# Kernel optimization log

Measured on AMD Instinct MI355X. Metric: run time of the kernel, lower is better.

The kernel has to match this reference:

```python
import jax, jax.numpy as jnp
import numpy as np

N_NODES = 50000
N_EDGES = 1600000
IN_DIM = 128
HEADS = 8
OUT_C = 16  # per-head channels; HEADS*OUT_C == IN_DIM -> residual active
NEG_SLOPE = 0.2
BN_EPS = 1e-5


def setup_inputs() -> dict:
    key = jax.random.key(0)
    ks = jax.random.split(key, 8)
    x = jax.random.normal(ks[0], (N_NODES, IN_DIM), dtype=jnp.float32)
    edge_index = jax.random.randint(ks[1], (2, N_EDGES), 0, N_NODES, dtype=jnp.int64)
    # GATConv params (PyG: shared lin for src/dst on single-tensor input)
    W = jax.random.normal(ks[2], (IN_DIM, HEADS * OUT_C), dtype=jnp.float32) / np.sqrt(IN_DIM)
    att_src = jax.random.normal(ks[3], (HEADS, OUT_C), dtype=jnp.float32) / np.sqrt(OUT_C)
    att_dst = jax.random.normal(ks[4], (HEADS, OUT_C), dtype=jnp.float32) / np.sqrt(OUT_C)
    bias = jnp.zeros((HEADS * OUT_C,), dtype=jnp.float32)
    # BatchNorm1d affine params
    gamma = jnp.ones((HEADS * OUT_C,), dtype=jnp.float32)
    beta = jnp.zeros((HEADS * OUT_C,), dtype=jnp.float32)
    return {"x": x, "edge_index": edge_index, "W": W, "att_src": att_src,
            "att_dst": att_dst, "bias": bias, "gamma": gamma, "beta": beta}


def reference(x, edge_index, W, att_src, att_dst, bias, gamma, beta):
    N = x.shape[0]
    H, C = att_src.shape
    src, dst = edge_index[0], edge_index[1]

    xl = (x @ W).reshape(N, H, C)                      # [N,H,C]
    a_src = jnp.sum(xl * att_src[None], axis=-1)       # [N,H]
    a_dst = jnp.sum(xl * att_dst[None], axis=-1)       # [N,H]

    e = jax.nn.leaky_relu(a_src[src] + a_dst[dst], NEG_SLOPE)  # [E,H]
    # segment softmax over incoming edges of each dst node
    m = jax.ops.segment_max(e, dst, num_segments=N)    # [N,H], -inf for empty
    m = jnp.where(jnp.isfinite(m), m, 0.0)
    ex = jnp.exp(e - m[dst])                           # [E,H]
    denom = jax.ops.segment_sum(ex, dst, num_segments=N)
    alpha = ex / (denom[dst] + 1e-16)                  # [E,H]

    out = jax.ops.segment_sum(alpha[:, :, None] * xl[src], dst, num_segments=N)  # [N,H,C]
    h = out.reshape(N, H * C) + bias

    # BatchNorm1d (training mode: batch statistics, biased variance)
    mean = jnp.mean(h, axis=0)
    var = jnp.mean((h - mean) ** 2, axis=0)
    h = (h - mean) * jax.lax.rsqrt(var + BN_EPS) * gamma + beta

    h = jax.nn.relu(h)
    return x + h  # residual (in_dim == H*C)
```

## Files before the change

kernel.cpp:

```cpp
#include <hip/hip_runtime.h>
#include <hip/hip_fp16.h>
#include <math.h>

#define N_NODES 50000
#define N_EDGES 1600000
#define DIM 128
#define HEADS 8
#define NEG_SLOPE 0.2f
#define BN_EPS 1e-5f

typedef _Float16 f16x8 __attribute__((ext_vector_type(8)));
typedef float f32x4 __attribute__((ext_vector_type(4)));

#define NBUCK 196
#define SEGCAP 12288
#define CHUNK 8192
#define NB_A ((N_EDGES + CHUNK - 1) / CHUNK)
#define LIN_NB ((N_NODES + 127) / 128)
#define FUSED_NB (NB_A + LIN_NB)

struct BinAShm {
    int hist[NBUCK], excl[NBUCK], gbase[NBUCK], cnt2[NBUCK];
    int sc[256];
    unsigned int buf[CHUNK];
};
struct LinShm { __half wh[16384]; };

__global__ __launch_bounds__(512) void k_linbinA(
        const float* __restrict__ x, const float* __restrict__ W,
        const float* __restrict__ att_s, const float* __restrict__ att_d,
        const int* __restrict__ ei, int* __restrict__ bcur,
        unsigned int* __restrict__ pairs, __half* __restrict__ xlh,
        float* __restrict__ a_src, float* __restrict__ a_dst) {
    __shared__ union { BinAShm a; LinShm l; } sh;
    const int t = threadIdx.x;

    if (blockIdx.x < NB_A) {
        const int base = blockIdx.x * CHUNK;
        const int cnt = min(CHUNK, N_EDGES - base);

        for (int j = t; j < NBUCK; j += 512) { sh.a.hist[j] = 0; sh.a.cnt2[j] = 0; }
        __syncthreads();
        for (int i = t * 4; i < cnt; i += 2048) {
            const int4 dv = *(const int4*)(ei + N_EDGES + base + i);
            atomicAdd(&sh.a.hist[dv.x >> 8], 1);
            atomicAdd(&sh.a.hist[dv.y >> 8], 1);
            atomicAdd(&sh.a.hist[dv.z >> 8], 1);
            atomicAdd(&sh.a.hist[dv.w >> 8], 1);
        }
        __syncthreads();
        if (t < 256) sh.a.sc[t] = (t < NBUCK) ? sh.a.hist[t] : 0;
        __syncthreads();
        for (int d = 1; d < 256; d <<= 1) {
            int xo = 0;
            if (t < 256 && t >= d) xo = sh.a.sc[t - d];
            __syncthreads();
            if (t < 256) sh.a.sc[t] += xo;
            __syncthreads();
        }
        if (t < NBUCK) {
            sh.a.excl[t] = sh.a.sc[t] - sh.a.hist[t];
            sh.a.gbase[t] = t * SEGCAP + atomicAdd(&bcur[t], sh.a.hist[t]);
        }
        __syncthreads();
        for (int i = t * 4; i < cnt; i += 2048) {
            const int4 sv = *(const int4*)(ei + base + i);
            const int4 dv = *(const int4*)(ei + N_EDGES + base + i);
            const int ss[4] = {sv.x, sv.y, sv.z, sv.w};
            const int dd[4] = {dv.x, dv.y, dv.z, dv.w};
            #pragma unroll
            for (int k = 0; k < 4; ++k) {
                const int b = dd[k] >> 8;
                const int r = atomicAdd(&sh.a.cnt2[b], 1);
                sh.a.buf[sh.a.excl[b] + r] = (unsigned int)ss[k]
                    | ((unsigned int)(dd[k] & 255) << 16) | ((unsigned int)b << 24);
            }
        }
        __syncthreads();
        for (int i = t; i < cnt; i += 512) {
            const unsigned int u = sh.a.buf[i];
            const int b = u >> 24;
            pairs[sh.a.gbase[b] + (i - sh.a.excl[b])] = u & 0xFFFFFF;
        }
    } else {
        for (int v = t; v < 2048; v += 512) {
            const int g = v >> 6, lane = v & 63;
            const int nt = g >> 2, kt = g & 3;
            const int q = lane >> 4, n = lane & 15;
            #pragma unroll
            for (int j = 0; j < 8; ++j)
                sh.l.wh[(size_t)(g * 64 + lane) * 8 + j] =
                    __float2half(W[(kt * 32 + q * 8 + j) * DIM + nt * 16 + n]);
        }
        __syncthreads();

        const int wave = t >> 6;
        const int lane = t & 63;
        const int q = lane >> 4, n = lane & 15;
        const int nb = ((blockIdx.x - NB_A) * 8 + wave) * 16;

        const int rowA = min(nb + n, N_NODES - 1);
        const float* xr = x + (size_t)rowA * DIM;
        f16x8 a[4];
        #pragma unroll
        for (int kt = 0; kt < 4; ++kt) {
            const float4 p0 = *(const float4*)(xr + kt * 32 + q * 8);
            const float4 p1 = *(const float4*)(xr + kt * 32 + q * 8 + 4);
            a[kt][0] = (_Float16)p0.x; a[kt][1] = (_Float16)p0.y;
            a[kt][2] = (_Float16)p0.z; a[kt][3] = (_Float16)p0.w;
            a[kt][4] = (_Float16)p1.x; a[kt][5] = (_Float16)p1.y;
            a[kt][6] = (_Float16)p1.z; a[kt][7] = (_Float16)p1.w;
        }

        f32x4 acc[8];
        #pragma unroll
        for (int nt = 0; nt < 8; ++nt) acc[nt] = (f32x4){0.f, 0.f, 0.f, 0.f};

        const f16x8* wb = (const f16x8*)sh.l.wh;
        #pragma unroll
        for (int nt = 0; nt < 8; ++nt) {
            #pragma unroll
            for (int kt = 0; kt < 4; ++kt) {
                const f16x8 b = wb[(nt * 4 + kt) * 64 + lane];
                acc[nt] = __builtin_amdgcn_mfma_f32_16x16x32_f16(a[kt], b, acc[nt], 0, 0, 0);
            }
        }

        const int r0 = nb + q * 4;
        #pragma unroll
        for (int nt = 0; nt < 8; ++nt) {
            const float as = att_s[nt * 16 + n];
            const float ad = att_d[nt * 16 + n];
            #pragma unroll
            for (int r = 0; r < 4; ++r) {
                const int row = r0 + r;
                const float v = acc[nt][r];
                float s = v * as;
                float d = v * ad;
                #pragma unroll
                for (int off = 8; off; off >>= 1) {
                    s += __shfl_xor(s, off, 16);
                    d += __shfl_xor(d, off, 16);
                }
                if (row < N_NODES) {
                    xlh[(size_t)row * DIM + nt * 16 + n] = __float2half(v);
                    if (n == 0) {
                        a_src[row * HEADS + nt] = s * 1.44269504f;
                        a_dst[row * HEADS + nt] = d * 1.44269504f;
                    }
                }
            }
        }
    }
}

__global__ __launch_bounds__(1024) void k_binB(const unsigned int* __restrict__ pairs,
                                               const int* __restrict__ bcur,
                                               unsigned short* __restrict__ csr,
                                               int2* __restrict__ nrange,
                                               float* __restrict__ gsums) {
    __shared__ int hist[256], eh[256], excl[256], cnt2[256];
    __shared__ int plen;
    __shared__ unsigned short out[SEGCAP];
    const int t = threadIdx.x;
    const int b = blockIdx.x;
    if (b == 0 && t < 256) gsums[t] = 0.f;
    const int lo = b * SEGCAP;
    const int cnt = bcur[b];

    if (t < 256) { hist[t] = 0; cnt2[t] = 0; }
    __syncthreads();
    for (int i = t; i < cnt; i += 1024)
        atomicAdd(&hist[pairs[lo + i] >> 16], 1);
    __syncthreads();
    if (t < 256) { eh[t] = (hist[t] + 1) & ~1; excl[t] = eh[t]; }
    __syncthreads();
    for (int d = 1; d < 256; d <<= 1) {
        int xo = 0;
        if (t < 256 && t >= d) xo = excl[t - d];
        __syncthreads();
        if (t < 256) excl[t] += xo;
        __syncthreads();
    }
    if (t < 256) excl[t] -= eh[t];
    if (t == 255) plen = excl[255] + eh[255];
    __syncthreads();
    for (int i = t; i < cnt; i += 1024) {
        const unsigned int u = pairs[lo + i];
        const int dl = u >> 16;
        const int r = atomicAdd(&cnt2[dl], 1);
        out[excl[dl] + r] = (unsigned short)(u & 0xFFFF);
    }
    __syncthreads();
    const int pl = plen;
    for (int i = t; i < pl; i += 1024)
        csr[2 * lo + i] = out[i];
    if (t < 256) {
        const int node = (b << 8) + t;
        if (node < N_NODES) {
            int2 rg;
            rg.x = 2 * lo + excl[t];
            rg.y = rg.x + hist[t];
            nrange[node] = rg;
        }
    }
}

#define AGG_NB (N_NODES / 4)

__global__ void k_aggr9(const int2* __restrict__ nrange,
                        const unsigned short* __restrict__ csr,
                        const float* __restrict__ a_src, const float* __restrict__ a_dst,
                        const __half* __restrict__ xlh, float* __restrict__ y) {
    const int d = blockIdx.x * 4 + (threadIdx.x >> 6);
    const int lane = threadIdx.x & 63;
    const int g = lane >> 4;
    const int cl = lane & 15;
    const int h = cl >> 1;
    const int2 rg = nrange[d];
    const int lo = rg.x, hi = rg.y;
    const float ad = a_dst[d * HEADS + h];

    float acc[8];
    #pragma unroll
    for (int k = 0; k < 8; ++k) acc[k] = 0.f;
    float dsum = 0.f;

    int i = lo;
    for (; i + 16 <= hi; i += 16) {
        const int s0 = csr[i + g];
        const int s1 = csr[i + 4 + g];
        const int s2 = csr[i + 8 + g];
        const int s3 = csr[i + 12 + g];
        const float as0 = a_src[s0 * HEADS + h];
        const float as1 = a_src[s1 * HEADS + h];
        const float as2 = a_src[s2 * HEADS + h];
        const float as3 = a_src[s3 * HEADS + h];
        const f16x8 x0 = *(const f16x8*)(xlh + (size_t)s0 * DIM + cl * 8);
        const f16x8 x1 = *(const f16x8*)(xlh + (size_t)s1 * DIM + cl * 8);
        const f16x8 x2 = *(const f16x8*)(xlh + (size_t)s2 * DIM + cl * 8);
        const f16x8 x3 = *(const f16x8*)(xlh + (size_t)s3 * DIM + cl * 8);
        const float e0 = as0 + ad;
        const float e1 = as1 + ad;
        const float e2 = as2 + ad;
        const float e3 = as3 + ad;
        const float w0 = exp2f(fmaxf(e0, NEG_SLOPE * e0));
        const float w1 = exp2f(fmaxf(e1, NEG_SLOPE * e1));
        const float w2 = exp2f(fmaxf(e2, NEG_SLOPE * e2));
        const float w3 = exp2f(fmaxf(e3, NEG_SLOPE * e3));
        dsum += (w0 + w1) + (w2 + w3);
        #pragma unroll
        for (int k = 0; k < 8; ++k) acc[k] = fmaf(w0, (float)x0[k], acc[k]);
        #pragma unroll
        for (int k = 0; k < 8; ++k) acc[k] = fmaf(w1, (float)x1[k], acc[k]);
        #pragma unroll
        for (int k = 0; k < 8; ++k) acc[k] = fmaf(w2, (float)x2[k], acc[k]);
        #pragma unroll
        for (int k = 0; k < 8; ++k) acc[k] = fmaf(w3, (float)x3[k], acc[k]);
    }
    for (; i + 8 <= hi; i += 8) {
        const int s0 = csr[i + g];
        const int s1 = csr[i + 4 + g];
        const float as0 = a_src[s0 * HEADS + h];
        const float as1 = a_src[s1 * HEADS + h];
        const f16x8 x0 = *(const f16x8*)(xlh + (size_t)s0 * DIM + cl * 8);
        const f16x8 x1 = *(const f16x8*)(xlh + (size_t)s1 * DIM + cl * 8);
        const float e0 = as0 + ad;
        const float e1 = as1 + ad;
        const float w0 = exp2f(fmaxf(e0, NEG_SLOPE * e0));
        const float w1 = exp2f(fmaxf(e1, NEG_SLOPE * e1));
        dsum += w0 + w1;
        #pragma unroll
        for (int k = 0; k < 8; ++k) acc[k] = fmaf(w0, (float)x0[k], acc[k]);
        #pragma unroll
        for (int k = 0; k < 8; ++k) acc[k] = fmaf(w1, (float)x1[k], acc[k]);
    }
    for (; i < hi; i += 4) {
        const int idx = i + g;
        const int sv = csr[min(idx, hi - 1)];
        const float e = a_src[sv * HEADS + h] + ad;
        const f16x8 xv = *(const f16x8*)(xlh + (size_t)sv * DIM + cl * 8);
        float w = exp2f(fmaxf(e, NEG_SLOPE * e));
        if (idx >= hi) w = 0.f;
        dsum += w;
        #pragma unroll
        for (int k = 0; k < 8; ++k) acc[k] = fmaf(w, (float)xv[k], acc[k]);
    }
    #pragma unroll
    for (int k = 0; k < 8; ++k) {
        acc[k] += __shfl_xor(acc[k], 16);
        acc[k] += __shfl_xor(acc[k], 32);
    }
    dsum += __shfl_xor(dsum, 16);
    dsum += __shfl_xor(dsum, 32);
    const float inv = 1.f / (dsum + 1e-16f);
    float2 o;
    o.x = acc[2 * g] * inv;
    o.y = acc[2 * g + 1] * inv;
    *(float2*)(y + (size_t)d * DIM + cl * 8 + g * 2) = o;
}

__global__ void k_stats(const float* __restrict__ y, const float* __restrict__ bias,
                        float* __restrict__ gsums) {
    const int c = threadIdx.x;
    const float b = bias[c];
    float s = 0.f, ss = 0.f;
    for (int n = blockIdx.x; n < N_NODES; n += gridDim.x) {
        const float h = y[n * DIM + c] + b;
        s += h;
        ss += h * h;
    }
    atomicAdd(&gsums[c], s);
    atomicAdd(&gsums[DIM + c], ss);
}

__global__ void k_final(float* __restrict__ y, const float* __restrict__ x,
                        const float* __restrict__ sums, const float* __restrict__ sumsq,
                        const float* __restrict__ gamma, const float* __restrict__ beta,
                        const float* __restrict__ bias) {
    const int q = blockIdx.x * blockDim.x + threadIdx.x;
    const int cq = q & (DIM / 4 - 1);
    const float4 sm = ((const float4*)sums)[cq];
    const float4 sq = ((const float4*)sumsq)[cq];
    const float4 gm = ((const float4*)gamma)[cq];
    const float4 bt = ((const float4*)beta)[cq];
    const float4 bs = ((const float4*)bias)[cq];
    float4 v = ((const float4*)y)[q];
    const float4 xv = ((const float4*)x)[q];
    const float inv_n = 1.f / (float)N_NODES;
#define BNC(c) { const float mean = sm.c * inv_n;                         \
                 const float var = sq.c * inv_n - mean * mean;            \
                 const float sc = rsqrtf(var + BN_EPS) * gm.c;            \
                 const float sh = bt.c + (bs.c - mean) * sc;              \
                 v.c = xv.c + fmaxf(v.c * sc + sh, 0.f); }
    BNC(x) BNC(y) BNC(z) BNC(w)
#undef BNC
    ((float4*)y)[q] = v;
}

extern "C" void kernel_launch(void* const* d_in, const int* in_sizes, int n_in,
                              void* d_out, int out_size, void* d_ws, size_t ws_size,
                              hipStream_t stream) {
    const float* x     = (const float*)d_in[0];
    const int*   ei    = (const int*)  d_in[1];
    const float* W     = (const float*)d_in[2];
    const float* att_s = (const float*)d_in[3];
    const float* att_d = (const float*)d_in[4];
    const float* bias  = (const float*)d_in[5];
    const float* gamma = (const float*)d_in[6];
    const float* beta  = (const float*)d_in[7];
    float* y = (float*)d_out;

    __half* xlh  = (__half*)d_ws;
    float* a_src = (float*)(xlh + (size_t)N_NODES * DIM);
    float* a_dst = a_src + (size_t)N_NODES * HEADS;
    float* sums  = a_dst + (size_t)N_NODES * HEADS;
    float* sumsq = sums  + DIM;
    int*   bcur  = (int*)(sumsq + DIM);
    int2*  nrange = (int2*)(bcur + 256);
    unsigned int* pairs = (unsigned int*)(nrange + N_NODES);
    unsigned short* csr = (unsigned short*)pairs;

    hipMemsetAsync(bcur, 0, 256 * sizeof(int), stream);
    k_linbinA<<<FUSED_NB, 512, 0, stream>>>(x, W, att_s, att_d, ei, bcur, pairs,
                                            xlh, a_src, a_dst);
    k_binB<<<NBUCK, 1024, 0, stream>>>(pairs, bcur, csr, nrange, sums);
    k_aggr9<<<AGG_NB, 256, 0, stream>>>(nrange, csr, a_src, a_dst, xlh, y);
    k_stats<<<512, DIM, 0, stream>>>(y, bias, sums);
    k_final<<<(size_t)N_NODES * DIM / 4 / 256, 256, 0, stream>>>(y, x, sums, sumsq,
                                                                 gamma, beta, bias);
}
```

Measured before the change: 229.2 us.

## Compute per-node degrees globally and scatter CSR directly without LDS staging

The bin-A pass now also counts per-destination degrees with global atomics. The second binning kernel uses those degrees and a bucket prefix scan to build a compact CSR, and scatters source ids straight to global memory through LDS cursors. This replaces the LDS histogram, the padded output buffer and the copy-out. In exchange it adds 1.6M global atomics, a larger memset, and uncoalesced global scatter writes. It also drops the even-padding of segments, which k_aggr9 may assume, and shrinks SEGCAP, which risks overflow if a bucket gets more edges than that.

```diff
diff --git a/kernel.cpp b/kernel.cpp
--- a/kernel.cpp
+++ b/kernel.cpp
@@ -13,7 +13,7 @@
 typedef float f32x4 __attribute__((ext_vector_type(4)));
 
 #define NBUCK 196
-#define SEGCAP 12288
+#define SEGCAP 9216
 #define CHUNK 8192
 #define NB_A ((N_EDGES + CHUNK - 1) / CHUNK)
 #define LIN_NB ((N_NODES + 127) / 128)
@@ -30,6 +30,7 @@
         const float* __restrict__ x, const float* __restrict__ W,
         const float* __restrict__ att_s, const float* __restrict__ att_d,
         const int* __restrict__ ei, int* __restrict__ bcur,
+        int* __restrict__ deg,
         unsigned int* __restrict__ pairs, __half* __restrict__ xlh,
         float* __restrict__ a_src, float* __restrict__ a_dst) {
     __shared__ union { BinAShm a; LinShm l; } sh;
@@ -47,6 +48,10 @@
             atomicAdd(&sh.a.hist[dv.y >> 8], 1);
             atomicAdd(&sh.a.hist[dv.z >> 8], 1);
             atomicAdd(&sh.a.hist[dv.w >> 8], 1);
+            atomicAdd(&deg[dv.x], 1);
+            atomicAdd(&deg[dv.y], 1);
+            atomicAdd(&deg[dv.z], 1);
+            atomicAdd(&deg[dv.w], 1);
         }
         __syncthreads();
         if (t < 256) sh.a.sc[t] = (t < NBUCK) ? sh.a.hist[t] : 0;
@@ -154,55 +159,61 @@
     }
 }
 
-__global__ __launch_bounds__(1024) void k_binB(const unsigned int* __restrict__ pairs,
+__global__ __launch_bounds__(512) void k_binB2(const unsigned int* __restrict__ pairs,
                                                const int* __restrict__ bcur,
+                                               const int* __restrict__ deg,
                                                unsigned short* __restrict__ csr,
                                                int2* __restrict__ nrange,
                                                float* __restrict__ gsums) {
-    __shared__ int hist[256], eh[256], excl[256], cnt2[256];
-    __shared__ int plen;
-    __shared__ unsigned short out[SEGCAP];
+    __shared__ int bsc[256];
+    __shared__ int dsc[256];
+    __shared__ int cur[256];
     const int t = threadIdx.x;
     const int b = blockIdx.x;
     if (b == 0 && t < 256) gsums[t] = 0.f;
-    const int lo = b * SEGCAP;
-    const int cnt = bcur[b];
-
-    if (t < 256) { hist[t] = 0; cnt2[t] = 0; }
-    __syncthreads();
-    for (int i = t; i < cnt; i += 1024)
-        atomicAdd(&hist[pairs[lo + i] >> 16], 1);
-    __syncthreads();
-    if (t < 256) { eh[t] = (hist[t] + 1) & ~1; excl[t] = eh[t]; }
+
+    if (t < 256) bsc[t] = (t < NBUCK) ? bcur[t] : 0;
     __syncthreads();
     for (int d = 1; d < 256; d <<= 1) {
         int xo = 0;
-        if (t < 256 && t >= d) xo = excl[t - d];
-        __syncthreads();
-        if (t < 256) excl[t] += xo;
-        __syncthreads();
-    }
-    if (t < 256) excl[t] -= eh[t];
-    if (t == 255) plen = excl[255] + eh[255];
+        if (t < 256 && t >= d) xo = bsc[t - d];
+        __syncthreads();
+        if (t < 256) bsc[t] += xo;
+        __syncthreads();
+    }
+    const int boff = (b == 0) ? 0 : bsc[b - 1];
+
+    int dg = 0;
+    const int node = (b << 8) + t;
+    if (t < 256) {
+        dg = (node < N_NODES) ? deg[node] : 0;
+        dsc[t] = dg;
+    }
     __syncthreads();
-    for (int i = t; i < cnt; i += 1024) {
+    for (int d = 1; d < 256; d <<= 1) {
+        int xo = 0;
+        if (t < 256 && t >= d) xo = dsc[t - d];
+        __syncthreads();
+        if (t < 256) dsc[t] += xo;
+        __syncthreads();
+    }
+    if (t < 256) {
+        const int start = boff + dsc[t] - dg;
+        if (node < N_NODES) {
+            int2 rg; rg.x = start; rg.y = start + dg;
+            nrange[node] = rg;
+        }
+        cur[t] = start;
+    }
+    __syncthreads();
+
+    const int cnt = bcur[b];
+    const int lo = b * SEGCAP;
+    for (int i = t; i < cnt; i += 512) {
         const unsigned int u = pairs[lo + i];
-        const int dl = u >> 16;
-        const int r = atomicAdd(&cnt2[dl], 1);
-        out[excl[dl] + r] = (unsigned short)(u & 0xFFFF);
-    }
-    __syncthreads();
-    const int pl = plen;
-    for (int i = t; i < pl; i += 1024)
-        csr[2 * lo + i] = out[i];
-    if (t < 256) {
-        const int node = (b << 8) + t;
-        if (node < N_NODES) {
-            int2 rg;
-            rg.x = 2 * lo + excl[t];
-            rg.y = rg.x + hist[t];
-            nrange[node] = rg;
-        }
+        const int dl = (u >> 16) & 255;
+        const int pos = atomicAdd(&cur[dl], 1);
+        csr[pos] = (unsigned short)(u & 0xFFFF);
     }
 }
 
@@ -356,15 +367,16 @@
     float* a_dst = a_src + (size_t)N_NODES * HEADS;
     float* sums  = a_dst + (size_t)N_NODES * HEADS;
     float* sumsq = sums  + DIM;
-    int*   bcur  = (int*)(sumsq + DIM);
+    int*   deg   = (int*)(sumsq + DIM);
+    int*   bcur  = deg + N_NODES;
     int2*  nrange = (int2*)(bcur + 256);
     unsigned int* pairs = (unsigned int*)(nrange + N_NODES);
-    unsigned short* csr = (unsigned short*)pairs;
-
-    hipMemsetAsync(bcur, 0, 256 * sizeof(int), stream);
-    k_linbinA<<<FUSED_NB, 512, 0, stream>>>(x, W, att_s, att_d, ei, bcur, pairs,
-                                            xlh, a_src, a_dst);
-    k_binB<<<NBUCK, 1024, 0, stream>>>(pairs, bcur, csr, nrange, sums);
+    unsigned short* csr = (unsigned short*)(pairs + (size_t)NBUCK * SEGCAP);
+
+    hipMemsetAsync(sums, 0, (size_t)(2 * DIM + N_NODES + 256) * sizeof(int), stream);
+    k_linbinA<<<FUSED_NB, 512, 0, stream>>>(x, W, att_s, att_d, ei, bcur, deg,
+                                            pairs, xlh, a_src, a_dst);
+    k_binB2<<<NBUCK, 512, 0, stream>>>(pairs, bcur, deg, csr, nrange, sums);
     k_aggr9<<<AGG_NB, 256, 0, stream>>>(nrange, csr, a_src, a_dst, xlh, y);
     k_stats<<<512, DIM, 0, stream>>>(y, bias, sums);
     k_final<<<(size_t)N_NODES * DIM / 4 / 256, 256, 0, stream>>>(y, x, sums, sumsq,
```

Result: slower. 288.8 us (+26.0%).

## Replace global bucket atomics with per-chunk metadata and split linear work across phases

Applied to the files above, without the earlier changes.

Binning pass A now writes each chunk's bucket-sorted pairs contiguously with per-chunk histogram/offset metadata, instead of scattering through global atomic cursors. Pass B gathers each bucket's pieces from all chunks via a prefix sum plus binary search. The memset and the global atomics go away. The linear/MFMA blocks are split across both phases so the second binning kernel overlaps with part of the GEMM work. The trade-off is extra metadata traffic, binary-search cost per edge in phase 2, and the lost CSR padding alignment.

```diff
diff --git a/kernel.cpp b/kernel.cpp
--- a/kernel.cpp
+++ b/kernel.cpp
@@ -17,29 +17,114 @@
 #define CHUNK 8192
 #define NB_A ((N_EDGES + CHUNK - 1) / CHUNK)
 #define LIN_NB ((N_NODES + 127) / 128)
-#define FUSED_NB (NB_A + LIN_NB)
+#define LIN_K1 195
+#define LIN_K2 (LIN_NB - LIN_K1)
+#define P1_NB (NB_A + LIN_K1)
+#define P2_NB (NBUCK + LIN_K2)
 
 struct BinAShm {
-    int hist[NBUCK], excl[NBUCK], gbase[NBUCK], cnt2[NBUCK];
+    int hist[NBUCK], excl[NBUCK], cnt2[NBUCK];
     int sc[256];
     unsigned int buf[CHUNK];
 };
+struct BinBShm {
+    int la[256], ea[256], rs[256];
+    int hist[256], excl[256], cnt2[256], sc[256];
+    unsigned short out[SEGCAP];
+};
 struct LinShm { __half wh[16384]; };
 
-__global__ __launch_bounds__(512) void k_linbinA(
+__device__ __forceinline__ void lin_block(
+        int linb, const float* __restrict__ x, const float* __restrict__ W,
+        const float* __restrict__ att_s, const float* __restrict__ att_d,
+        __half* __restrict__ xlh, float* __restrict__ a_src,
+        float* __restrict__ a_dst, __half* wh) {
+    const int t = threadIdx.x;
+    for (int v = t; v < 2048; v += 512) {
+        const int g = v >> 6, lane = v & 63;
+        const int nt = g >> 2, kt = g & 3;
+        const int q = lane >> 4, n = lane & 15;
+        #pragma unroll
+        for (int j = 0; j < 8; ++j)
+            wh[(size_t)(g * 64 + lane) * 8 + j] =
+                __float2half(W[(kt * 32 + q * 8 + j) * DIM + nt * 16 + n]);
+    }
+    __syncthreads();
+
+    const int wave = t >> 6;
+    const int lane = t & 63;
+    const int q = lane >> 4, n = lane & 15;
+    const int nb = (linb * 8 + wave) * 16;
+
+    const int rowA = min(nb + n, N_NODES - 1);
+    const float* xr = x + (size_t)rowA * DIM;
+    f16x8 a[4];
+    #pragma unroll
+    for (int kt = 0; kt < 4; ++kt) {
+        const float4 p0 = *(const float4*)(xr + kt * 32 + q * 8);
+        const float4 p1 = *(const float4*)(xr + kt * 32 + q * 8 + 4);
+        a[kt][0] = (_Float16)p0.x; a[kt][1] = (_Float16)p0.y;
+        a[kt][2] = (_Float16)p0.z; a[kt][3] = (_Float16)p0.w;
+        a[kt][4] = (_Float16)p1.x; a[kt][5] = (_Float16)p1.y;
+        a[kt][6] = (_Float16)p1.z; a[kt][7] = (_Float16)p1.w;
+    }
+
+    f32x4 acc[8];
+    #pragma unroll
+    for (int nt = 0; nt < 8; ++nt) acc[nt] = (f32x4){0.f, 0.f, 0.f, 0.f};
+
+    const f16x8* wb = (const f16x8*)wh;
+    #pragma unroll
+    for (int nt = 0; nt < 8; ++nt) {
+        #pragma unroll
+        for (int kt = 0; kt < 4; ++kt) {
+            const f16x8 b = wb[(nt * 4 + kt) * 64 + lane];
+            acc[nt] = __builtin_amdgcn_mfma_f32_16x16x32_f16(a[kt], b, acc[nt], 0, 0, 0);
+        }
+    }
+
+    const int r0 = nb + q * 4;
+    #pragma unroll
+    for (int nt = 0; nt < 8; ++nt) {
+        const float as = att_s[nt * 16 + n];
+        const float ad = att_d[nt * 16 + n];
+        #pragma unroll
+        for (int r = 0; r < 4; ++r) {
+            const int row = r0 + r;
+            const float v = acc[nt][r];
+            float s = v * as;
+            float d = v * ad;
+            #pragma unroll
+            for (int off = 8; off; off >>= 1) {
+                s += __shfl_xor(s, off, 16);
+                d += __shfl_xor(d, off, 16);
+            }
+            if (row < N_NODES) {
+                xlh[(size_t)row * DIM + nt * 16 + n] = __float2half(v);
+                if (n == 0) {
+                    a_src[row * HEADS + nt] = s * 1.44269504f;
+                    a_dst[row * HEADS + nt] = d * 1.44269504f;
+                }
+            }
+        }
+    }
+}
+
+__global__ __launch_bounds__(512) void k_phase1(
         const float* __restrict__ x, const float* __restrict__ W,
         const float* __restrict__ att_s, const float* __restrict__ att_d,
-        const int* __restrict__ ei, int* __restrict__ bcur,
+        const int* __restrict__ ei, unsigned int* __restrict__ meta,
         unsigned int* __restrict__ pairs, __half* __restrict__ xlh,
         float* __restrict__ a_src, float* __restrict__ a_dst) {
     __shared__ union { BinAShm a; LinShm l; } sh;
     const int t = threadIdx.x;
 
     if (blockIdx.x < NB_A) {
-        const int base = blockIdx.x * CHUNK;
+        const int blk = blockIdx.x;
+        const int base = blk * CHUNK;
         const int cnt = min(CHUNK, N_EDGES - base);
 
-        for (int j = t; j < NBUCK; j += 512) { sh.a.hist[j] = 0; sh.a.cnt2[j] = 0; }
+        if (t < NBUCK) { sh.a.hist[t] = 0; sh.a.cnt2[t] = 0; }
         __syncthreads();
         for (int i = t * 4; i < cnt; i += 2048) {
             const int4 dv = *(const int4*)(ei + N_EDGES + base + i);
@@ -59,8 +144,10 @@
             __syncthreads();
         }
         if (t < NBUCK) {
-            sh.a.excl[t] = sh.a.sc[t] - sh.a.hist[t];
-            sh.a.gbase[t] = t * SEGCAP + atomicAdd(&bcur[t], sh.a.hist[t]);
+            const int ex = sh.a.sc[t] - sh.a.hist[t];
+            sh.a.excl[t] = ex;
+            meta[(size_t)blk * NBUCK + t] =
+                (unsigned int)sh.a.hist[t] | ((unsigned int)ex << 16);
         }
         __syncthreads();
         for (int i = t * 4; i < cnt; i += 2048) {
@@ -73,136 +160,102 @@
                 const int b = dd[k] >> 8;
                 const int r = atomicAdd(&sh.a.cnt2[b], 1);
                 sh.a.buf[sh.a.excl[b] + r] = (unsigned int)ss[k]
-                    | ((unsigned int)(dd[k] & 255) << 16) | ((unsigned int)b << 24);
-            }
-        }
-        __syncthreads();
+                    | ((unsigned int)(dd[k] & 255) << 16);
+            }
+        }
+        __syncthreads();
+        for (int i = t * 4; i < cnt; i += 2048)
+            *(int4*)(pairs + base + i) = *(const int4*)(sh.a.buf + i);
+    } else {
+        lin_block(blockIdx.x - NB_A, x, W, att_s, att_d, xlh, a_src, a_dst, sh.l.wh);
+    }
+}
+
+__global__ __launch_bounds__(512) void k_phase2(
+        const unsigned int* __restrict__ pairs, const unsigned int* __restrict__ meta,
+        unsigned short* __restrict__ csr, int2* __restrict__ nrange,
+        float* __restrict__ gsums,
+        const float* __restrict__ x, const float* __restrict__ W,
+        const float* __restrict__ att_s, const float* __restrict__ att_d,
+        __half* __restrict__ xlh, float* __restrict__ a_src,
+        float* __restrict__ a_dst) {
+    __shared__ union { BinBShm b; LinShm l; } sh;
+    const int t = threadIdx.x;
+
+    if (blockIdx.x < NBUCK) {
+        const int b = blockIdx.x;
+        if (b == 0 && t < 256) gsums[t] = 0.f;
+
+        if (t < 256) {
+            int len = 0, off = 0;
+            if (t < NB_A) {
+                const unsigned int m = meta[(size_t)t * NBUCK + b];
+                len = (int)(m & 0xFFFF);
+                off = (int)(m >> 16);
+            }
+            sh.b.la[t] = len; sh.b.ea[t] = off; sh.b.rs[t] = len;
+            sh.b.hist[t] = 0; sh.b.cnt2[t] = 0;
+        }
+        __syncthreads();
+        for (int d = 1; d < 256; d <<= 1) {
+            int xo = 0;
+            if (t < 256 && t >= d) xo = sh.b.rs[t - d];
+            __syncthreads();
+            if (t < 256) sh.b.rs[t] += xo;
+            __syncthreads();
+        }
+        const int cnt = sh.b.rs[NB_A - 1];
+
         for (int i = t; i < cnt; i += 512) {
-            const unsigned int u = sh.a.buf[i];
-            const int b = u >> 24;
-            pairs[sh.a.gbase[b] + (i - sh.a.excl[b])] = u & 0xFFFFFF;
+            int loa = 0, hia = NB_A - 1;
+            while (loa < hia) {
+                const int mid = (loa + hia) >> 1;
+                if (sh.b.rs[mid] > i) hia = mid; else loa = mid + 1;
+            }
+            const int j = i - (sh.b.rs[loa] - sh.b.la[loa]);
+            const unsigned int u = pairs[(size_t)loa * CHUNK + sh.b.ea[loa] + j];
+            atomicAdd(&sh.b.hist[(u >> 16) & 255], 1);
+        }
+        __syncthreads();
+        if (t < 256) sh.b.sc[t] = sh.b.hist[t];
+        __syncthreads();
+        for (int d = 1; d < 256; d <<= 1) {
+            int xo = 0;
+            if (t < 256 && t >= d) xo = sh.b.sc[t - d];
+            __syncthreads();
+            if (t < 256) sh.b.sc[t] += xo;
+            __syncthreads();
+        }
+        if (t < 256) sh.b.excl[t] = sh.b.sc[t] - sh.b.hist[t];
+        __syncthreads();
+
+        for (int i = t; i < cnt; i += 512) {
+            int loa = 0, hia = NB_A - 1;
+            while (loa < hia) {
+                const int mid = (loa + hia) >> 1;
+                if (sh.b.rs[mid] > i) hia = mid; else loa = mid + 1;
+            }
+            const int j = i - (sh.b.rs[loa] - sh.b.la[loa]);
+            const unsigned int u = pairs[(size_t)loa * CHUNK + sh.b.ea[loa] + j];
+            const int dl = (u >> 16) & 255;
+            const int r = atomicAdd(&sh.b.cnt2[dl], 1);
+            sh.b.out[sh.b.excl[dl] + r] = (unsigned short)(u & 0xFFFF);
+        }
+        __syncthreads();
+        for (int i = t; i < cnt; i += 512)
+            csr[(size_t)b * SEGCAP + i] = sh.b.out[i];
+        if (t < 256) {
+            const int node = (b << 8) + t;
+            if (node < N_NODES) {
+                int2 rg;
+                rg.x = b * SEGCAP + sh.b.excl[t];
+                rg.y = rg.x + sh.b.hist[t];
+                nrange[node] = rg;
+            }
         }
     } else {
-        for (int v = t; v < 2048; v += 512) {
-            const int g = v >> 6, lane = v & 63;
-            const int nt = g >> 2, kt = g & 3;
-            const int q = lane >> 4, n = lane & 15;
-            #pragma unroll
-            for (int j = 0; j < 8; ++j)
-                sh.l.wh[(size_t)(g * 64 + lane) * 8 + j] =
-                    __float2half(W[(kt * 32 + q * 8 + j) * DIM + nt * 16 + n]);
-        }
-        __syncthreads();
-
-        const int wave = t >> 6;
-        const int lane = t & 63;
-        const int q = lane >> 4, n = lane & 15;
-        const int nb = ((blockIdx.x - NB_A) * 8 + wave) * 16;
-
-        const int rowA = min(nb + n, N_NODES - 1);
-        const float* xr = x + (size_t)rowA * DIM;
-        f16x8 a[4];
-        #pragma unroll
-        for (int kt = 0; kt < 4; ++kt) {
-            const float4 p0 = *(const float4*)(xr + kt * 32 + q * 8);
-            const float4 p1 = *(const float4*)(xr + kt * 32 + q * 8 + 4);
-            a[kt][0] = (_Float16)p0.x; a[kt][1] = (_Float16)p0.y;
-            a[kt][2] = (_Float16)p0.z; a[kt][3] = (_Float16)p0.w;
-            a[kt][4] = (_Float16)p1.x; a[kt][5] = (_Float16)p1.y;
-            a[kt][6] = (_Float16)p1.z; a[kt][7] = (_Float16)p1.w;
-        }
-
-        f32x4 acc[8];
-        #pragma unroll
-        for (int nt = 0; nt < 8; ++nt) acc[nt] = (f32x4){0.f, 0.f, 0.f, 0.f};
-
-        const f16x8* wb = (const f16x8*)sh.l.wh;
-        #pragma unroll
-        for (int nt = 0; nt < 8; ++nt) {
-            #pragma unroll
-            for (int kt = 0; kt < 4; ++kt) {
-                const f16x8 b = wb[(nt * 4 + kt) * 64 + lane];
-                acc[nt] = __builtin_amdgcn_mfma_f32_16x16x32_f16(a[kt], b, acc[nt], 0, 0, 0);
-            }
-        }
-
-        const int r0 = nb + q * 4;
-        #pragma unroll
-        for (int nt = 0; nt < 8; ++nt) {
-            const float as = att_s[nt * 16 + n];
-            const float ad = att_d[nt * 16 + n];
-            #pragma unroll
-            for (int r = 0; r < 4; ++r) {
-                const int row = r0 + r;
-                const float v = acc[nt][r];
-                float s = v * as;
-                float d = v * ad;
-                #pragma unroll
-                for (int off = 8; off; off >>= 1) {
-                    s += __shfl_xor(s, off, 16);
-                    d += __shfl_xor(d, off, 16);
-                }
-                if (row < N_NODES) {
-                    xlh[(size_t)row * DIM + nt * 16 + n] = __float2half(v);
-                    if (n == 0) {
-                        a_src[row * HEADS + nt] = s * 1.44269504f;
-                        a_dst[row * HEADS + nt] = d * 1.44269504f;
-                    }
-                }
-            }
-        }
-    }
-}
-
-__global__ __launch_bounds__(1024) void k_binB(const unsigned int* __restrict__ pairs,
-                                               const int* __restrict__ bcur,
-                                               unsigned short* __restrict__ csr,
-                                               int2* __restrict__ nrange,
-                                               float* __restrict__ gsums) {
-    __shared__ int hist[256], eh[256], excl[256], cnt2[256];
-    __shared__ int plen;
-    __shared__ unsigned short out[SEGCAP];
-    const int t = threadIdx.x;
-    const int b = blockIdx.x;
-    if (b == 0 && t < 256) gsums[t] = 0.f;
-    const int lo = b * SEGCAP;
-    const int cnt = bcur[b];
-
-    if (t < 256) { hist[t] = 0; cnt2[t] = 0; }
-    __syncthreads();
-    for (int i = t; i < cnt; i += 1024)
-        atomicAdd(&hist[pairs[lo + i] >> 16], 1);
-    __syncthreads();
-    if (t < 256) { eh[t] = (hist[t] + 1) & ~1; excl[t] = eh[t]; }
-    __syncthreads();
-    for (int d = 1; d < 256; d <<= 1) {
-        int xo = 0;
-        if (t < 256 && t >= d) xo = excl[t - d];
-        __syncthreads();
-        if (t < 256) excl[t] += xo;
-        __syncthreads();
-    }
-    if (t < 256) excl[t] -= eh[t];
-    if (t == 255) plen = excl[255] + eh[255];
-    __syncthreads();
-    for (int i = t; i < cnt; i += 1024) {
-        const unsigned int u = pairs[lo + i];
-        const int dl = u >> 16;
-        const int r = atomicAdd(&cnt2[dl], 1);
-        out[excl[dl] + r] = (unsigned short)(u & 0xFFFF);
-    }
-    __syncthreads();
-    const int pl = plen;
-    for (int i = t; i < pl; i += 1024)
-        csr[2 * lo + i] = out[i];
-    if (t < 256) {
-        const int node = (b << 8) + t;
-        if (node < N_NODES) {
-            int2 rg;
-            rg.x = 2 * lo + excl[t];
-            rg.y = rg.x + hist[t];
-            nrange[node] = rg;
-        }
+        lin_block(LIN_K1 + (int)blockIdx.x - NBUCK, x, W, att_s, att_d,
+                  xlh, a_src, a_dst, sh.l.wh);
     }
 }
 
@@ -356,15 +409,15 @@
     float* a_dst = a_src + (size_t)N_NODES * HEADS;
     float* sums  = a_dst + (size_t)N_NODES * HEADS;
     float* sumsq = sums  + DIM;
-    int*   bcur  = (int*)(sumsq + DIM);
-    int2*  nrange = (int2*)(bcur + 256);
-    unsigned int* pairs = (unsigned int*)(nrange + N_NODES);
-    unsigned short* csr = (unsigned short*)pairs;
-
-    hipMemsetAsync(bcur, 0, 256 * sizeof(int), stream);
-    k_linbinA<<<FUSED_NB, 512, 0, stream>>>(x, W, att_s, att_d, ei, bcur, pairs,
-                                            xlh, a_src, a_dst);
-    k_binB<<<NBUCK, 1024, 0, stream>>>(pairs, bcur, csr, nrange, sums);
+    int2*  nrange = (int2*)(sumsq + DIM);
+    unsigned int* meta  = (unsigned int*)(nrange + N_NODES);
+    unsigned int* pairs = meta + (size_t)NB_A * NBUCK;
+    unsigned short* csr = (unsigned short*)(pairs + (size_t)NB_A * CHUNK);
+
+    k_phase1<<<P1_NB, 512, 0, stream>>>(x, W, att_s, att_d, ei, meta, pairs,
+                                        xlh, a_src, a_dst);
+    k_phase2<<<P2_NB, 512, 0, stream>>>(pairs, meta, csr, nrange, sums,
+                                        x, W, att_s, att_d, xlh, a_src, a_dst);
     k_aggr9<<<AGG_NB, 256, 0, stream>>>(nrange, csr, a_src, a_dst, xlh, y);
     k_stats<<<512, DIM, 0, stream>>>(y, bias, sums);
     k_final<<<(size_t)N_NODES * DIM / 4 / 256, 256, 0, stream>>>(y, x, sums, sumsq,
```

Measured after the change: 241.1 us. 1.05x slower.

## Split aggregation into two launches and spread BN stat atomics over replica banks

Applied to the files above, without the earlier changes.

The single aggregation launch is split into two half-size launches on the same stream, each covering half the destination nodes through a base-offset argument. The BatchNorm statistics atomics are spread across 8 replicated accumulator banks to reduce contention, and a new single-block kernel sums the banks before the final normalization. The bank zeroing moves into binB to cover the larger buffer. This adds two extra kernel launches and their overhead in exchange for less atomic contention, and the aggregation split gives no clear benefit.

```diff
diff --git a/kernel.cpp b/kernel.cpp
--- a/kernel.cpp
+++ b/kernel.cpp
@@ -158,13 +158,13 @@
                                                const int* __restrict__ bcur,
                                                unsigned short* __restrict__ csr,
                                                int2* __restrict__ nrange,
-                                               float* __restrict__ gsums) {
+                                               float* __restrict__ grep) {
     __shared__ int hist[256], eh[256], excl[256], cnt2[256];
     __shared__ int plen;
     __shared__ unsigned short out[SEGCAP];
     const int t = threadIdx.x;
     const int b = blockIdx.x;
-    if (b == 0 && t < 256) gsums[t] = 0.f;
+    if (b == 0) { for (int j = t; j < 2048; j += 1024) grep[j] = 0.f; }
     const int lo = b * SEGCAP;
     const int cnt = bcur[b];
 
@@ -206,13 +206,14 @@
     }
 }
 
-#define AGG_NB (N_NODES / 4)
+#define AGG_HALF_NB (N_NODES / 8)
 
 __global__ void k_aggr9(const int2* __restrict__ nrange,
                         const unsigned short* __restrict__ csr,
                         const float* __restrict__ a_src, const float* __restrict__ a_dst,
-                        const __half* __restrict__ xlh, float* __restrict__ y) {
-    const int d = blockIdx.x * 4 + (threadIdx.x >> 6);
+                        const __half* __restrict__ xlh, float* __restrict__ y,
+                        int nbase) {
+    const int d = nbase + blockIdx.x * 4 + (threadIdx.x >> 6);
     const int lane = threadIdx.x & 63;
     const int g = lane >> 4;
     const int cl = lane & 15;
@@ -301,17 +302,26 @@
 }
 
 __global__ void k_stats(const float* __restrict__ y, const float* __restrict__ bias,
-                        float* __restrict__ gsums) {
+                        float* __restrict__ grep) {
     const int c = threadIdx.x;
     const float b = bias[c];
+    float* bank = grep + (blockIdx.x & 7) * 256;
     float s = 0.f, ss = 0.f;
     for (int n = blockIdx.x; n < N_NODES; n += gridDim.x) {
         const float h = y[n * DIM + c] + b;
         s += h;
         ss += h * h;
     }
-    atomicAdd(&gsums[c], s);
-    atomicAdd(&gsums[DIM + c], ss);
+    atomicAdd(&bank[c], s);
+    atomicAdd(&bank[DIM + c], ss);
+}
+
+__global__ void k_red(const float* __restrict__ grep, float* __restrict__ gred) {
+    const int j = threadIdx.x;
+    float v = 0.f;
+    #pragma unroll
+    for (int r = 0; r < 8; ++r) v += grep[r * 256 + j];
+    gred[j] = v;
 }
 
 __global__ void k_final(float* __restrict__ y, const float* __restrict__ x,
@@ -354,9 +364,9 @@
     __half* xlh  = (__half*)d_ws;
     float* a_src = (float*)(xlh + (size_t)N_NODES * DIM);
     float* a_dst = a_src + (size_t)N_NODES * HEADS;
-    float* sums  = a_dst + (size_t)N_NODES * HEADS;
-    float* sumsq = sums  + DIM;
-    int*   bcur  = (int*)(sumsq + DIM);
+    float* gred  = a_dst + (size_t)N_NODES * HEADS;
+    float* grep  = gred + 256;
+    int*   bcur  = (int*)(grep + 2048);
     int2*  nrange = (int2*)(bcur + 256);
     unsigned int* pairs = (unsigned int*)(nrange + N_NODES);
     unsigned short* csr = (unsigned short*)pairs;
@@ -364,9 +374,13 @@
     hipMemsetAsync(bcur, 0, 256 * sizeof(int), stream);
     k_linbinA<<<FUSED_NB, 512, 0, stream>>>(x, W, att_s, att_d, ei, bcur, pairs,
                                             xlh, a_src, a_dst);
-    k_binB<<<NBUCK, 1024, 0, stream>>>(pairs, bcur, csr, nrange, sums);
-    k_aggr9<<<AGG_NB, 256, 0, stream>>>(nrange, csr, a_src, a_dst, xlh, y);
-    k_stats<<<512, DIM, 0, stream>>>(y, bias, sums);
-    k_final<<<(size_t)N_NODES * DIM / 4 / 256, 256, 0, stream>>>(y, x, sums, sumsq,
+    k_binB<<<NBUCK, 1024, 0, stream>>>(pairs, bcur, csr, nrange, grep);
+    k_aggr9<<<AGG_HALF_NB, 256, 0, stream>>>(nrange, csr, a_src, a_dst, xlh, y, 0);
+    k_aggr9<<<AGG_HALF_NB, 256, 0, stream>>>(nrange, csr, a_src, a_dst, xlh, y,
+                                             N_NODES / 2);
+    k_stats<<<512, DIM, 0, stream>>>(y, bias, grep);
+    k_red<<<1, 256, 0, stream>>>(grep, gred);
+    k_final<<<(size_t)N_NODES * DIM / 4 / 256, 256, 0, stream>>>(y, x, gred,
+                                                                 gred + DIM,
                                                                  gamma, beta, bias);
 }
```

Result: no change. 226.5 us (-1.2%).
